# Optimization experiments

Hardware: AMD Instinct MI355X
Metric: run time of the kernel (lower is better)

The kernel has to match this reference:

```python
import jax, jax.numpy as jnp
import numpy as np

B, N, E, H = 4, 2048, 288, 8
D = E // H  # head_dim = 36


def setup_inputs() -> dict:
    key = jax.random.key(0)
    ks = jax.random.split(key, 8)
    s = 1.0 / np.sqrt(E)
    return {
        "query": jax.random.normal(ks[0], (B, N, E), jnp.float32),
        "key": jax.random.normal(ks[1], (B, N, E), jnp.float32),
        "value": jax.random.normal(ks[2], (B, N, E), jnp.float32),
        "Wq": jax.random.normal(ks[3], (E, E), jnp.float32) * s,
        "bq": jnp.zeros((E,), jnp.float32),
        "Wk": jax.random.normal(ks[4], (E, E), jnp.float32) * s,
        "bk": jnp.zeros((E,), jnp.float32),
        "Wv": jax.random.normal(ks[5], (E, E), jnp.float32) * s,
        "bv": jnp.zeros((E,), jnp.float32),
        "Wo": jax.random.normal(ks[6], (E, E), jnp.float32) * s,
        "bo": jnp.zeros((E,), jnp.float32),
    }


def reference(query, key, value, Wq, bq, Wk, bk, Wv, bv, Wo, bo):
    scaling = float(D) ** (-0.5)
    q = (query @ Wq + bq) * scaling            # (B, N, E), pre-scaled as in source
    k = key @ Wk + bk                          # (B, N, E)
    v = value @ Wv + bv                        # (B, N, E)
    # split heads: per-head slices along last dim == reshape to (B, N, H, D)
    qh = q.reshape(B, N, H, D)
    kh = k.reshape(B, N, H, D)
    vh = v.reshape(B, N, H, D)
    scores = jnp.einsum("bnhd,bmhd->bhnm", qh, kh)   # (B, H, N, N)
    attn = jax.nn.softmax(scores, axis=-1)
    out = jnp.einsum("bhnm,bmhd->bnhd", attn, vh)    # (B, N, H, D)
    out = out.reshape(B, N, E)                       # concat heads
    return out @ Wo + bo
```

## Files before the change

kernel.cpp:

```cpp
#include <hip/hip_runtime.h>

#define E 288
#define NSEQ 2048
#define BATCH 4
#define NH 8
#define HD 36
#define BH (BATCH * NH)
#define ROWS (BATCH * NSEQ)
#define BHN (BH * NSEQ)

typedef _Float16 half8_t __attribute__((ext_vector_type(8)));
typedef _Float16 half4_t __attribute__((ext_vector_type(4)));
typedef float f32x4 __attribute__((ext_vector_type(4)));
typedef int i32x4 __attribute__((ext_vector_type(4)));

__device__ __forceinline__ int sw64(int row, int col) {
  return (row << 6) + ((((col >> 3) ^ row) & 7) << 3) + (col & 7);
}

__device__ __forceinline__ int toff(int r, int k) {
  const int rp = r >> 1;
  const int g = (((r & 1) << 2) + (k >> 3)) ^ (rp & 7);
  return (rp << 6) + ((g & 7) << 3) + (k & 7);
}

__device__ __forceinline__ void gld16(const _Float16* g, _Float16* l) {
  __builtin_amdgcn_global_load_lds(
      (const __attribute__((address_space(1))) void*)g,
      (__attribute__((address_space(3))) void*)l, 16, 0, 0);
}

__device__ __forceinline__ float fexp2(float x) {
  return __builtin_amdgcn_exp2f(x);
}

#define XBLK 6912
#define WBLK 1296
#define QZBLK 2048

__global__ __launch_bounds__(256) void prep_kernel(
    const float* __restrict__ xq, const float* __restrict__ xk,
    const float* __restrict__ xv, const float* __restrict__ Wq,
    const float* __restrict__ Wk, const float* __restrict__ Wv,
    const float* __restrict__ Wo, _Float16* __restrict__ x16blk,
    _Float16* __restrict__ wblk, _Float16* __restrict__ q16) {
  const int bid = blockIdx.x;
  const int tid = threadIdx.x;
  if (bid < XBLK) {
    const int i = bid * 256 + tid;
    const int mode = i / (ROWS * 72);
    const int rem = i - mode * (ROWS * 72);
    const int row = rem / 72, k4 = rem - row * 72;
    const float* x = (mode == 0) ? xq : (mode == 1) ? xk : xv;
    const float4 v = *(const float4*)&x[(size_t)row * E + k4 * 4];
    half4_t h = {(_Float16)v.x, (_Float16)v.y, (_Float16)v.z, (_Float16)v.w};
    _Float16* dst = x16blk + (size_t)mode * (64 * 9 * 4096) +
                    ((((row >> 7) * 9 + (k4 >> 3))) << 12) +
                    toff(row & 127, (k4 & 7) * 4);
    *(half4_t*)dst = h;
  } else if (bid < XBLK + WBLK) {
    const int j = (bid - XBLK) * 256 + tid;
    const int m = j / (E * E);
    const int rem = j - m * (E * E);
    const int k = rem / E, n = rem - k * E;
    const float* W = (m == 0) ? Wq : (m == 1) ? Wk : (m == 2) ? Wv : Wo;
    wblk[(size_t)((m * 3 + n / 96) * 9 + (k >> 5)) * 3072 +
         toff(n % 96, k & 31)] = (_Float16)W[(size_t)k * E + n];
  } else {
    const int j = (bid - XBLK - WBLK) * 256 + tid;
    ((i32x4*)q16)[j] = (i32x4){0, 0, 0, 0};
  }
}

#define PM 128
#define PN 96

struct QKVArgs {
  const _Float16* x[3];
  const float* bias[3];
  _Float16* out[3];
};

__global__ __launch_bounds__(256, 4) void proj_qkv_kernel(
    QKVArgs A, const _Float16* __restrict__ wblk) {
  __shared__ __align__(16) _Float16 abuf[2][4096];
  __shared__ __align__(16) _Float16 wbuf[2][3072];

  const int tid = threadIdx.x;
  const int lane = tid & 63, w = tid >> 6;
  const int quad = lane >> 4, l15 = lane & 15;
  const int mode = blockIdx.z;
  const int RB = blockIdx.x, CT = blockIdx.y;
  const _Float16* __restrict__ ablk = A.x[mode] + (size_t)RB * 9 * 4096;
  const _Float16* __restrict__ wb = wblk + (size_t)(mode * 3 + CT) * 9 * 3072;

  f32x4 acc[2][6];
#pragma unroll
  for (int t = 0; t < 2; ++t)
#pragma unroll
    for (int nt = 0; nt < 6; ++nt) acc[t][nt] = (f32x4){0.f, 0.f, 0.f, 0.f};

#pragma unroll
  for (int seg = w; seg < 8; seg += 4)
    gld16(ablk + seg * 512 + lane * 8, abuf[0] + seg * 512);
  for (int seg = w; seg < 6; seg += 4)
    gld16(wb + seg * 512 + lane * 8, wbuf[0] + seg * 512);

  for (int C = 0; C < 9; ++C) {
    const int cur = C & 1;
    __syncthreads();
    if (C + 1 < 9) {
#pragma unroll
      for (int seg = w; seg < 8; seg += 4)
        gld16(ablk + (C + 1) * 4096 + seg * 512 + lane * 8,
              abuf[cur ^ 1] + seg * 512);
      for (int seg = w; seg < 6; seg += 4)
        gld16(wb + (C + 1) * 3072 + seg * 512 + lane * 8,
              wbuf[cur ^ 1] + seg * 512);
    }
    half8_t ah[2];
#pragma unroll
    for (int t = 0; t < 2; ++t)
      ah[t] = *(const half8_t*)&abuf[cur][toff(w * 32 + t * 16 + l15, quad * 8)];
#pragma unroll
    for (int nt = 0; nt < 6; ++nt) {
      const half8_t bf = *(const half8_t*)&wbuf[cur][toff(nt * 16 + l15, quad * 8)];
#pragma unroll
      for (int t = 0; t < 2; ++t)
        acc[t][nt] = __builtin_amdgcn_mfma_f32_16x16x32_f16(ah[t], bf, acc[t][nt], 0, 0, 0);
    }
  }

  const float* __restrict__ bias = A.bias[mode];
  _Float16* __restrict__ outp = A.out[mode];
  const float scale = (mode == 0) ? 0.24044917348149868f : 1.0f;
  const int row0 = RB * PM, col0 = CT * PN;
#pragma unroll
  for (int nt = 0; nt < 6; ++nt) {
    const int col = col0 + nt * 16 + l15;
    const int h = col / 36, d = col - h * 36;
    const float bc = bias[col];
#pragma unroll
    for (int t = 0; t < 2; ++t) {
#pragma unroll
      for (int r = 0; r < 4; ++r) {
        const int row = row0 + w * 32 + t * 16 + quad * 4 + r;
        const int b = row >> 11, n = row & (NSEQ - 1);
        const int bh = b * NH + h;
        const _Float16 val = (_Float16)((acc[t][nt][r] + bc) * scale);
        if (mode == 0) {
          outp[((size_t)bh * NSEQ + n) * 64 + d] = val;
        } else {
          const int kt = n >> 6, c = n & 63;
          if (mode == 1) {
            outp[((size_t)bh * 32 + kt) * 4096 + sw64(c, d)] = val;
          } else {
            const int pc = ((c & 15) << 2) | (c >> 4);
            outp[((size_t)bh * 32 + kt) * 3072 + sw64(d, pc)] = val;
          }
        }
      }
    }
  }
}

#define QB 128
#define KT 64
#define SPLIT 4

__device__ __forceinline__ void stage_tile(const _Float16* kg, const _Float16* vg,
                                           _Float16* kb, _Float16* vb, int w,
                                           int lane) {
#pragma unroll
  for (int seg = w; seg < 8; seg += 4)
    gld16(kg + seg * 512 + lane * 8, kb + seg * 512);
  for (int seg = w; seg < 6; seg += 4)
    gld16(vg + seg * 512 + lane * 8, vb + seg * 512);
}

__global__ __launch_bounds__(256, 3) void attn_kernel(
    const _Float16* __restrict__ q16, const _Float16* __restrict__ kblk,
    const _Float16* __restrict__ vblk, _Float16* __restrict__ pacc16,
    float* __restrict__ psum) {
  __shared__ __align__(16) _Float16 kbuf[2][KT * 64];
  __shared__ __align__(16) _Float16 vbuf[2][48 * 64];
  __shared__ __align__(16) _Float16 pbuf[QB * 64];

  const int tid = threadIdx.x;
  const int lane = tid & 63;
  const int w = tid >> 6;
  const int quad = lane >> 4;
  const int l15 = lane & 15;

  const int id = blockIdx.x;
  const int xcd = id & 7;
  const int qb = (id >> 3) & 15;
  const int g = id >> 7;
  const int bhc = g * 8 + xcd;
  const int bh = bhc >> 2;
  const int chunk = bhc & 3;
  const int q0 = qb * QB;

  const _Float16* qbase = q16 + ((size_t)bh * NSEQ + q0 + w * 32) * 64;
  half8_t qf[2][2];
#pragma unroll
  for (int t = 0; t < 2; ++t)
#pragma unroll
    for (int kc = 0; kc < 2; ++kc)
      qf[t][kc] = *(const half8_t*)&qbase[(t * 16 + l15) * 64 + kc * 32 + quad * 8];

  f32x4 oacc[2][3];
#pragma unroll
  for (int t = 0; t < 2; ++t)
#pragma unroll
    for (int nt = 0; nt < 3; ++nt) oacc[t][nt] = (f32x4){0.f, 0.f, 0.f, 0.f};
  float ssum[2][4] = {{0.f, 0.f, 0.f, 0.f}, {0.f, 0.f, 0.f, 0.f}};

  const int t0 = chunk * 8;
  const _Float16* kbase = kblk + ((size_t)bh * 32 + t0) * 4096;
  const _Float16* vbase = vblk + ((size_t)bh * 32 + t0) * 3072;

  stage_tile(kbase, vbase, kbuf[0], vbuf[0], w, lane);

  for (int it = 0; it < 8; ++it) {
    const int cur = it & 1;
    __syncthreads();
    if (it + 1 < 8)
      stage_tile(kbase + (it + 1) * 4096, vbase + (it + 1) * 3072,
                 kbuf[cur ^ 1], vbuf[cur ^ 1], w, lane);

#pragma unroll
    for (int t = 0; t < 2; ++t) {
      f32x4 sc[4];
#pragma unroll
      for (int s = 0; s < 4; ++s) {
        const half8_t kf0 = *(const half8_t*)&kbuf[cur][sw64(s * 16 + l15, quad * 8)];
        const half8_t kf1 = *(const half8_t*)&kbuf[cur][sw64(s * 16 + l15, 32 + quad * 8)];
        f32x4 c0 = __builtin_amdgcn_mfma_f32_16x16x32_f16(
            qf[t][0], kf0, (f32x4){0.f, 0.f, 0.f, 0.f}, 0, 0, 0);
        sc[s] = __builtin_amdgcn_mfma_f32_16x16x32_f16(qf[t][1], kf1, c0, 0, 0, 0);
      }
#pragma unroll
      for (int r = 0; r < 4; ++r) {
        const float p0 = fexp2(sc[0][r]);
        const float p1 = fexp2(sc[1][r]);
        const float p2 = fexp2(sc[2][r]);
        const float p3 = fexp2(sc[3][r]);
        ssum[t][r] += (p0 + p1) + (p2 + p3);
        half4_t ph = {(_Float16)p0, (_Float16)p1, (_Float16)p2, (_Float16)p3};
        *(half4_t*)&pbuf[sw64(w * 32 + t * 16 + quad * 4 + r, l15 * 4)] = ph;
      }
    }

#pragma unroll
    for (int kc = 0; kc < 2; ++kc) {
      half8_t vf[3];
#pragma unroll
      for (int nt = 0; nt < 3; ++nt)
        vf[nt] = *(const half8_t*)&vbuf[cur][sw64(nt * 16 + l15, kc * 32 + quad * 8)];
#pragma unroll
      for (int t = 0; t < 2; ++t) {
        const half8_t af = *(const half8_t*)&pbuf[sw64(w * 32 + t * 16 + l15, kc * 32 + quad * 8)];
#pragma unroll
        for (int nt = 0; nt < 3; ++nt)
          oacc[t][nt] = __builtin_amdgcn_mfma_f32_16x16x32_f16(af, vf[nt], oacc[t][nt], 0, 0, 0);
      }
    }
  }

#pragma unroll
  for (int t = 0; t < 2; ++t) {
#pragma unroll
    for (int r = 0; r < 4; ++r) {
      float s = ssum[t][r];
      s += __shfl_xor(s, 1);
      s += __shfl_xor(s, 2);
      s += __shfl_xor(s, 4);
      s += __shfl_xor(s, 8);
      const int row = q0 + w * 32 + t * 16 + quad * 4 + r;
      const size_t gr = (size_t)chunk * BHN + (size_t)bh * NSEQ + row;
      if (l15 == 0) psum[gr] = s;
#pragma unroll
      for (int nt = 0; nt < 3; ++nt) {
        const int col = nt * 16 + l15;
        if (col < HD) pacc16[gr * HD + col] = (_Float16)oacc[t][nt][r];
      }
    }
  }
}

__global__ __launch_bounds__(256) void combine_kernel(
    const _Float16* __restrict__ pacc16, const float* __restrict__ psum,
    _Float16* __restrict__ abh, _Float16* __restrict__ abl) {
  const int idx = blockIdx.x * 256 + threadIdx.x;
  if (idx >= BHN * 9) return;
  const int gr = idx / 9;
  const int d4 = idx - gr * 9;

  float a[4] = {0.f, 0.f, 0.f, 0.f};
  float s = 0.f;
#pragma unroll
  for (int c = 0; c < SPLIT; ++c) {
    const half4_t p = *(const half4_t*)&pacc16[((size_t)c * BHN + gr) * HD + d4 * 4];
#pragma unroll
    for (int j = 0; j < 4; ++j) a[j] += (float)p[j];
    s += psum[(size_t)c * BHN + gr];
  }
  const float inv = 1.0f / s;
  const int bh = gr >> 11;
  const int n = gr & (NSEQ - 1);
  const int b = bh >> 3, h = bh & 7;
  const int row = b * NSEQ + n;
  const int col = h * 36 + d4 * 4;

  half4_t hv, lv;
#pragma unroll
  for (int j = 0; j < 4; ++j) {
    const float val = a[j] * inv;
    const _Float16 hi = (_Float16)val;
    hv[j] = hi;
    lv[j] = (_Float16)(val - (float)hi);
  }
  const size_t o = (size_t)((row >> 6) * 9 + (col >> 5)) * 2048 + toff(row & 63, col & 31);
  *(half4_t*)&abh[o] = hv;
  *(half4_t*)&abl[o] = lv;
}

__global__ __launch_bounds__(256, 4) void proj_o_kernel(
    const _Float16* __restrict__ abh, const _Float16* __restrict__ abl,
    const _Float16* __restrict__ wblk_o, const float* __restrict__ bias,
    float* __restrict__ out) {
  __shared__ __align__(16) _Float16 hbuf[2][2048];
  __shared__ __align__(16) _Float16 lbuf[2][2048];
  __shared__ __align__(16) _Float16 wbuf[2][3072];

  const int tid = threadIdx.x;
  const int lane = tid & 63, w = tid >> 6;
  const int quad = lane >> 4, l15 = lane & 15;
  const int RB = blockIdx.x, CT = blockIdx.y;
  const _Float16* __restrict__ hblk = abh + (size_t)RB * 9 * 2048;
  const _Float16* __restrict__ lblk = abl + (size_t)RB * 9 * 2048;
  const _Float16* __restrict__ wb = wblk_o + (size_t)CT * 9 * 3072;

  f32x4 acc[6];
#pragma unroll
  for (int nt = 0; nt < 6; ++nt) acc[nt] = (f32x4){0.f, 0.f, 0.f, 0.f};

  gld16(hblk + w * 512 + lane * 8, hbuf[0] + w * 512);
  gld16(lblk + w * 512 + lane * 8, lbuf[0] + w * 512);
  for (int seg = w; seg < 6; seg += 4)
    gld16(wb + seg * 512 + lane * 8, wbuf[0] + seg * 512);

  for (int C = 0; C < 9; ++C) {
    const int cur = C & 1;
    __syncthreads();
    if (C + 1 < 9) {
      gld16(hblk + (C + 1) * 2048 + w * 512 + lane * 8, hbuf[cur ^ 1] + w * 512);
      gld16(lblk + (C + 1) * 2048 + w * 512 + lane * 8, lbuf[cur ^ 1] + w * 512);
      for (int seg = w; seg < 6; seg += 4)
        gld16(wb + (C + 1) * 3072 + seg * 512 + lane * 8, wbuf[cur ^ 1] + seg * 512);
    }
    const half8_t ah = *(const half8_t*)&hbuf[cur][toff(w * 16 + l15, quad * 8)];
    const half8_t al = *(const half8_t*)&lbuf[cur][toff(w * 16 + l15, quad * 8)];
#pragma unroll
    for (int nt = 0; nt < 6; ++nt) {
      const half8_t bf = *(const half8_t*)&wbuf[cur][toff(nt * 16 + l15, quad * 8)];
      acc[nt] = __builtin_amdgcn_mfma_f32_16x16x32_f16(ah, bf, acc[nt], 0, 0, 0);
      acc[nt] = __builtin_amdgcn_mfma_f32_16x16x32_f16(al, bf, acc[nt], 0, 0, 0);
    }
  }

#pragma unroll
  for (int nt = 0; nt < 6; ++nt) {
    const int col = CT * PN + nt * 16 + l15;
    const float bc = bias[col];
#pragma unroll
    for (int r = 0; r < 4; ++r) {
      const int row = RB * 64 + w * 16 + quad * 4 + r;
      out[(size_t)row * E + col] = acc[nt][r] + bc;
    }
  }
}

extern "C" void kernel_launch(void* const* d_in, const int* in_sizes, int n_in,
                              void* d_out, int out_size, void* d_ws,
                              size_t ws_size, hipStream_t stream) {
  const float* query = (const float*)d_in[0];
  const float* key_ = (const float*)d_in[1];
  const float* value = (const float*)d_in[2];
  const float* Wq = (const float*)d_in[3];
  const float* bq = (const float*)d_in[4];
  const float* Wk = (const float*)d_in[5];
  const float* bk = (const float*)d_in[6];
  const float* Wv = (const float*)d_in[7];
  const float* bv = (const float*)d_in[8];
  const float* Wo = (const float*)d_in[9];
  const float* bo = (const float*)d_in[10];
  float* out = (float*)d_out;

  _Float16* q16 = (_Float16*)d_ws;
  _Float16* kblk = q16 + (size_t)BH * NSEQ * 64;
  _Float16* vblk = kblk + (size_t)BH * 32 * 4096;
  _Float16* x16blk = vblk + (size_t)BH * 32 * 3072;
  _Float16* wblk = x16blk + (size_t)3 * 64 * 9 * 4096;
  _Float16* abh = wblk + (size_t)4 * 3 * 9 * 3072;
  _Float16* abl = abh + (size_t)128 * 9 * 2048;
  _Float16* pacc16 = abl + (size_t)128 * 9 * 2048;
  float* psum = (float*)(pacc16 + (size_t)SPLIT * BHN * HD);

  prep_kernel<<<XBLK + WBLK + QZBLK, 256, 0, stream>>>(
      query, key_, value, Wq, Wk, Wv, Wo, x16blk, wblk, q16);

  QKVArgs qa;
  qa.x[0] = x16blk + 0 * (size_t)(64 * 9 * 4096);
  qa.x[1] = x16blk + 1 * (size_t)(64 * 9 * 4096);
  qa.x[2] = x16blk + 2 * (size_t)(64 * 9 * 4096);
  qa.bias[0] = bq; qa.bias[1] = bk; qa.bias[2] = bv;
  qa.out[0] = q16; qa.out[1] = kblk; qa.out[2] = vblk;
  proj_qkv_kernel<<<dim3(ROWS / PM, E / PN, 3), 256, 0, stream>>>(qa, wblk);

  attn_kernel<<<dim3((NSEQ / QB) * BH * SPLIT), 256, 0, stream>>>(
      q16, kblk, vblk, pacc16, psum);

  combine_kernel<<<(BHN * 9) / 256, 256, 0, stream>>>(pacc16, psum, abh, abl);

  proj_o_kernel<<<dim3(ROWS / 64, E / PN), 256, 0, stream>>>(
      abh, abl, wblk + (size_t)3 * 3 * 9 * 3072, bo, out);
}
```

Measured before the change: 172.8 us.

## Fuse fp32-to-fp16 input conversion into QKV projection and shrink attention P buffer

The prep pass that converted the fp32 query/key/value activations into a tiled fp16 workspace is removed. The QKV projection now loads fp32 rows directly through registers, converts them, and writes them into swizzled LDS, prefetching two chunks ahead. This drops a full write and re-read of the converted activations. The attention kernel's P buffer shrinks to one 16-row tile per wave, with the PV MFMAs interleaved per row tile and V fragments hoisted, and launch bounds rise to 4 blocks per CU for occupancy. The trade-off is register-staged A loads in place of direct global-to-LDS loads, plus more register pressure under the higher occupancy target.

Measured after the change: 169.7 us. About the same (-1.8%).

```diff
diff --git a/kernel.cpp b/kernel.cpp
--- a/kernel.cpp
+++ b/kernel.cpp
@@ -34,32 +34,17 @@
   return __builtin_amdgcn_exp2f(x);
 }
 
-#define XBLK 6912
 #define WBLK 1296
 #define QZBLK 2048
 
 __global__ __launch_bounds__(256) void prep_kernel(
-    const float* __restrict__ xq, const float* __restrict__ xk,
-    const float* __restrict__ xv, const float* __restrict__ Wq,
-    const float* __restrict__ Wk, const float* __restrict__ Wv,
-    const float* __restrict__ Wo, _Float16* __restrict__ x16blk,
+    const float* __restrict__ Wq, const float* __restrict__ Wk,
+    const float* __restrict__ Wv, const float* __restrict__ Wo,
     _Float16* __restrict__ wblk, _Float16* __restrict__ q16) {
   const int bid = blockIdx.x;
   const int tid = threadIdx.x;
-  if (bid < XBLK) {
-    const int i = bid * 256 + tid;
-    const int mode = i / (ROWS * 72);
-    const int rem = i - mode * (ROWS * 72);
-    const int row = rem / 72, k4 = rem - row * 72;
-    const float* x = (mode == 0) ? xq : (mode == 1) ? xk : xv;
-    const float4 v = *(const float4*)&x[(size_t)row * E + k4 * 4];
-    half4_t h = {(_Float16)v.x, (_Float16)v.y, (_Float16)v.z, (_Float16)v.w};
-    _Float16* dst = x16blk + (size_t)mode * (64 * 9 * 4096) +
-                    ((((row >> 7) * 9 + (k4 >> 3))) << 12) +
-                    toff(row & 127, (k4 & 7) * 4);
-    *(half4_t*)dst = h;
-  } else if (bid < XBLK + WBLK) {
-    const int j = (bid - XBLK) * 256 + tid;
+  if (bid < WBLK) {
+    const int j = bid * 256 + tid;
     const int m = j / (E * E);
     const int rem = j - m * (E * E);
     const int k = rem / E, n = rem - k * E;
@@ -67,7 +52,7 @@
     wblk[(size_t)((m * 3 + n / 96) * 9 + (k >> 5)) * 3072 +
          toff(n % 96, k & 31)] = (_Float16)W[(size_t)k * E + n];
   } else {
-    const int j = (bid - XBLK - WBLK) * 256 + tid;
+    const int j = (bid - WBLK) * 256 + tid;
     ((i32x4*)q16)[j] = (i32x4){0, 0, 0, 0};
   }
 }
@@ -76,7 +61,7 @@
 #define PN 96
 
 struct QKVArgs {
-  const _Float16* x[3];
+  const float* x[3];
   const float* bias[3];
   _Float16* out[3];
 };
@@ -91,8 +76,27 @@
   const int quad = lane >> 4, l15 = lane & 15;
   const int mode = blockIdx.z;
   const int RB = blockIdx.x, CT = blockIdx.y;
-  const _Float16* __restrict__ ablk = A.x[mode] + (size_t)RB * 9 * 4096;
+  const float* __restrict__ x = A.x[mode];
   const _Float16* __restrict__ wb = wblk + (size_t)(mode * 3 + CT) * 9 * 3072;
+  const int row0 = RB * PM;
+
+  float4 apre[4];
+  auto loadA = [&](int C) {
+#pragma unroll
+    for (int iu = 0; iu < 4; ++iu) {
+      const int i = tid + 256 * iu, r = i >> 3, c4 = i & 7;
+      apre[iu] = *(const float4*)&x[(size_t)(row0 + r) * E + C * 32 + c4 * 4];
+    }
+  };
+  auto writeA = [&](_Float16* dst) {
+#pragma unroll
+    for (int iu = 0; iu < 4; ++iu) {
+      const int i = tid + 256 * iu, r = i >> 3, c4 = i & 7;
+      half4_t h = {(_Float16)apre[iu].x, (_Float16)apre[iu].y,
+                   (_Float16)apre[iu].z, (_Float16)apre[iu].w};
+      *(half4_t*)&dst[toff(r, c4 * 4)] = h;
+    }
+  };
 
   f32x4 acc[2][6];
 #pragma unroll
@@ -100,23 +104,21 @@
 #pragma unroll
     for (int nt = 0; nt < 6; ++nt) acc[t][nt] = (f32x4){0.f, 0.f, 0.f, 0.f};
 
-#pragma unroll
-  for (int seg = w; seg < 8; seg += 4)
-    gld16(ablk + seg * 512 + lane * 8, abuf[0] + seg * 512);
+  loadA(0);
+  writeA(abuf[0]);
   for (int seg = w; seg < 6; seg += 4)
     gld16(wb + seg * 512 + lane * 8, wbuf[0] + seg * 512);
+  loadA(1);
 
   for (int C = 0; C < 9; ++C) {
     const int cur = C & 1;
     __syncthreads();
     if (C + 1 < 9) {
-#pragma unroll
-      for (int seg = w; seg < 8; seg += 4)
-        gld16(ablk + (C + 1) * 4096 + seg * 512 + lane * 8,
-              abuf[cur ^ 1] + seg * 512);
       for (int seg = w; seg < 6; seg += 4)
         gld16(wb + (C + 1) * 3072 + seg * 512 + lane * 8,
               wbuf[cur ^ 1] + seg * 512);
+      writeA(abuf[cur ^ 1]);
+      if (C + 2 < 9) loadA(C + 2);
     }
     half8_t ah[2];
 #pragma unroll
@@ -134,7 +136,7 @@
   const float* __restrict__ bias = A.bias[mode];
   _Float16* __restrict__ outp = A.out[mode];
   const float scale = (mode == 0) ? 0.24044917348149868f : 1.0f;
-  const int row0 = RB * PM, col0 = CT * PN;
+  const int col0 = CT * PN;
 #pragma unroll
   for (int nt = 0; nt < 6; ++nt) {
     const int col = col0 + nt * 16 + l15;
@@ -178,13 +180,13 @@
     gld16(vg + seg * 512 + lane * 8, vb + seg * 512);
 }
 
-__global__ __launch_bounds__(256, 3) void attn_kernel(
+__global__ __launch_bounds__(256, 4) void attn_kernel(
     const _Float16* __restrict__ q16, const _Float16* __restrict__ kblk,
     const _Float16* __restrict__ vblk, _Float16* __restrict__ pacc16,
     float* __restrict__ psum) {
   __shared__ __align__(16) _Float16 kbuf[2][KT * 64];
   __shared__ __align__(16) _Float16 vbuf[2][48 * 64];
-  __shared__ __align__(16) _Float16 pbuf[QB * 64];
+  __shared__ __align__(16) _Float16 pbuf[4][16 * 64];
 
   const int tid = threadIdx.x;
   const int lane = tid & 63;
@@ -229,6 +231,13 @@
       stage_tile(kbase + (it + 1) * 4096, vbase + (it + 1) * 3072,
                  kbuf[cur ^ 1], vbuf[cur ^ 1], w, lane);
 
+    half8_t vf[2][3];
+#pragma unroll
+    for (int kc = 0; kc < 2; ++kc)
+#pragma unroll
+      for (int nt = 0; nt < 3; ++nt)
+        vf[kc][nt] = *(const half8_t*)&vbuf[cur][sw64(nt * 16 + l15, kc * 32 + quad * 8)];
+
 #pragma unroll
     for (int t = 0; t < 2; ++t) {
       f32x4 sc[4];
@@ -248,22 +257,14 @@
         const float p3 = fexp2(sc[3][r]);
         ssum[t][r] += (p0 + p1) + (p2 + p3);
         half4_t ph = {(_Float16)p0, (_Float16)p1, (_Float16)p2, (_Float16)p3};
-        *(half4_t*)&pbuf[sw64(w * 32 + t * 16 + quad * 4 + r, l15 * 4)] = ph;
+        *(half4_t*)&pbuf[w][sw64(quad * 4 + r, l15 * 4)] = ph;
       }
-    }
-
-#pragma unroll
-    for (int kc = 0; kc < 2; ++kc) {
-      half8_t vf[3];
-#pragma unroll
-      for (int nt = 0; nt < 3; ++nt)
-        vf[nt] = *(const half8_t*)&vbuf[cur][sw64(nt * 16 + l15, kc * 32 + quad * 8)];
-#pragma unroll
-      for (int t = 0; t < 2; ++t) {
-        const half8_t af = *(const half8_t*)&pbuf[sw64(w * 32 + t * 16 + l15, kc * 32 + quad * 8)];
+#pragma unroll
+      for (int kc = 0; kc < 2; ++kc) {
+        const half8_t af = *(const half8_t*)&pbuf[w][sw64(l15, kc * 32 + quad * 8)];
 #pragma unroll
         for (int nt = 0; nt < 3; ++nt)
-          oacc[t][nt] = __builtin_amdgcn_mfma_f32_16x16x32_f16(af, vf[nt], oacc[t][nt], 0, 0, 0);
+          oacc[t][nt] = __builtin_amdgcn_mfma_f32_16x16x32_f16(af, vf[kc][nt], oacc[t][nt], 0, 0, 0);
       }
     }
   }
@@ -401,20 +402,16 @@
   _Float16* q16 = (_Float16*)d_ws;
   _Float16* kblk = q16 + (size_t)BH * NSEQ * 64;
   _Float16* vblk = kblk + (size_t)BH * 32 * 4096;
-  _Float16* x16blk = vblk + (size_t)BH * 32 * 3072;
-  _Float16* wblk = x16blk + (size_t)3 * 64 * 9 * 4096;
+  _Float16* wblk = vblk + (size_t)BH * 32 * 3072;
   _Float16* abh = wblk + (size_t)4 * 3 * 9 * 3072;
   _Float16* abl = abh + (size_t)128 * 9 * 2048;
   _Float16* pacc16 = abl + (size_t)128 * 9 * 2048;
   float* psum = (float*)(pacc16 + (size_t)SPLIT * BHN * HD);
 
-  prep_kernel<<<XBLK + WBLK + QZBLK, 256, 0, stream>>>(
-      query, key_, value, Wq, Wk, Wv, Wo, x16blk, wblk, q16);
+  prep_kernel<<<WBLK + QZBLK, 256, 0, stream>>>(Wq, Wk, Wv, Wo, wblk, q16);
 
   QKVArgs qa;
-  qa.x[0] = x16blk + 0 * (size_t)(64 * 9 * 4096);
-  qa.x[1] = x16blk + 1 * (size_t)(64 * 9 * 4096);
-  qa.x[2] = x16blk + 2 * (size_t)(64 * 9 * 4096);
+  qa.x[0] = query; qa.x[1] = key_; qa.x[2] = value;
   qa.bias[0] = bq; qa.bias[1] = bk; qa.bias[2] = bv;
   qa.out[0] = q16; qa.out[1] = kblk; qa.out[2] = vblk;
   proj_qkv_kernel<<<dim3(ROWS / PM, E / PN, 3), 256, 0, stream>>>(qa, wblk);
```
